# Kernel optimization log

Hardware: AMD Instinct MI355X
Metric: run time of the kernel (lower is better)

Reference implementation:

```python
import jax, jax.numpy as jnp
import numpy as np
from jax import lax

IN_FEATURES = 8192
OUT_FEATURES = 28672


def _unpack3(qweight, infeatures):
    """Unpack GPTQ-style 3-bit weights.

    qweight: (infeatures//32*3, O) int32. Every 3 consecutive int32 rows hold
    32 packed 3-bit values per column (GPTQ quant.py packing): values 0-9 in
    word0 bits [0..30), value 10 split over word0[30:32]|word1[0:1],
    values 11-20 in word1 bits [1..31), value 21 split over word1[31:32]|word2[0:2],
    values 22-31 in word2 bits [2..32).
    Returns float32 (infeatures, O) with raw quant codes in [0, 8).
    """
    O = qweight.shape[1]
    G = infeatures // 32
    q = lax.bitcast_convert_type(qweight, jnp.uint32).reshape(G, 3, O)
    w0, w1, w2 = q[:, 0], q[:, 1], q[:, 2]
    sh = jnp.arange(10, dtype=jnp.uint32)  # 10 whole values per word
    v0 = (w0[:, None, :] >> (3 * sh)[None, :, None]) & 7          # (G,10,O)
    v10 = (((w0 >> 30) & 3) | ((w1 & 1) << 2))[:, None, :]        # (G,1,O)
    v1 = (w1[:, None, :] >> (3 * sh + 1)[None, :, None]) & 7       # (G,10,O)
    v21 = (((w1 >> 31) & 1) | ((w2 & 3) << 1))[:, None, :]        # (G,1,O)
    v2 = (w2[:, None, :] >> (3 * sh + 2)[None, :, None]) & 7       # (G,10,O)
    vals = jnp.concatenate([v0, v10, v1, v21, v2], axis=1)        # (G,32,O)
    return vals.reshape(infeatures, O).astype(jnp.float32)


def setup_inputs() -> dict:
    key = jax.random.key(0)
    k1, k2, k3, k4, k5 = jax.random.split(key, 5)
    x = jax.random.normal(k1, (1, IN_FEATURES), dtype=jnp.float32)
    qweight = jax.random.randint(k2, (IN_FEATURES // 32 * 3, OUT_FEATURES), 0, 2147483647, dtype=jnp.int32)
    scales = jax.random.uniform(k3, (OUT_FEATURES, 1), dtype=jnp.float32)
    zeros = jax.random.normal(k4, (OUT_FEATURES, 1), dtype=jnp.float32)
    bias = jax.random.normal(k5, (OUT_FEATURES,), dtype=jnp.float32)
    return {"x": x, "qweight": qweight, "scales": scales, "zeros": zeros, "bias": bias}


def reference(x, qweight, scales, zeros, bias):
    infeatures = x.shape[-1]
    q = _unpack3(qweight, infeatures)            # (K, O) float codes
    # per-output-channel dequant: W[k, o] = scales[o] * q[k, o] - zeros[o]
    W = scales.T * q - zeros.T                   # (K, O)
    y = x @ W + bias                             # (1, O)
    return y
```

## Files before the change

kernel.cpp:

```cpp
#include <hip/hip_runtime.h>
#include <stdint.h>


typedef float v2f __attribute__((ext_vector_type(2)));

constexpr int O_FEAT  = 28672;
constexpr int IN_FEAT = 8192;
constexpr int NGROUP  = IN_FEAT / 32;
constexpr int SPLIT   = 32;
constexpr int GPB     = NGROUP / SPLIT;
constexpr int O4      = O_FEAT / 4;

__device__ __forceinline__ void dot_group_pk(uint32_t w0, uint32_t w1, uint32_t w2,
                                             const v2f xv[16], v2f& acc) {
  v2f a0 = acc, a1 = {0.f, 0.f};
  #pragma unroll
  for (int t = 0; t < 5; ++t) {
    v2f q = { (float)((w0 >> (6 * t)) & 7u), (float)((w0 >> (6 * t + 3)) & 7u) };
    (t & 1 ? a1 : a0) += xv[t] * q;
  }
  {
    v2f q = { (float)((w0 >> 30) | ((w1 & 1u) << 2)), (float)((w1 >> 1) & 7u) };
    a1 += xv[5] * q;
  }
  #pragma unroll
  for (int t = 0; t < 4; ++t) {
    v2f q = { (float)((w1 >> (4 + 6 * t)) & 7u), (float)((w1 >> (7 + 6 * t)) & 7u) };
    (t & 1 ? a1 : a0) += xv[6 + t] * q;
  }
  {
    v2f q = { (float)((w1 >> 28) & 7u), (float)((w1 >> 31) | ((w2 & 3u) << 1)) };
    a0 += xv[10] * q;
  }
  #pragma unroll
  for (int t = 0; t < 5; ++t) {
    v2f q = { (float)((w2 >> (2 + 6 * t)) & 7u), (float)((w2 >> (5 + 6 * t)) & 7u) };
    (t & 1 ? a1 : a0) += xv[11 + t] * q;
  }
  acc = a0 + a1;
}

__global__ __launch_bounds__(64) void q3_partial(const float* __restrict__ x,
                                                 const uint4* __restrict__ qw4,
                                                 float* __restrict__ part,
                                                 float* __restrict__ partS) {
  const int tcol4 = blockIdx.x * 64 + threadIdx.x;
  const int g0    = blockIdx.y * GPB;
  const uint4* qp = qw4 + (size_t)(3 * g0) * O4 + tcol4;

  __shared__ float xs[GPB * 32];
  const float4 xt = reinterpret_cast<const float4*>(x + g0 * 32)[threadIdx.x];
  reinterpret_cast<float4*>(xs)[threadIdx.x] = xt;

  if (blockIdx.x == 0) {
    float s = (xt.x + xt.y) + (xt.z + xt.w);
    #pragma unroll
    for (int off = 32; off > 0; off >>= 1) s += __shfl_down(s, off, 64);
    if (threadIdx.x == 0) partS[blockIdx.y] = s;
  }

  v2f acc0 = {0.f, 0.f}, acc1 = {0.f, 0.f}, acc2 = {0.f, 0.f}, acc3 = {0.f, 0.f};

  uint4 na = qp[0], nb = qp[O4], nc = qp[2 * O4];
  for (int g = 0; g < GPB; ++g) {
    const uint4 wa = na, wb = nb, wc = nc;
    qp += (g < GPB - 1) ? 3 * O4 : 0;
    na = qp[0]; nb = qp[O4]; nc = qp[2 * O4];

    v2f xv[16];
    const float4* s4 = reinterpret_cast<const float4*>(&xs[g * 32]);
    #pragma unroll
    for (int u = 0; u < 8; ++u) {
      float4 t = s4[u];
      xv[2 * u]     = v2f{t.x, t.y};
      xv[2 * u + 1] = v2f{t.z, t.w};
    }

    dot_group_pk(wa.x, wb.x, wc.x, xv, acc0);
    dot_group_pk(wa.y, wb.y, wc.y, xv, acc1);
    dot_group_pk(wa.z, wb.z, wc.z, xv, acc2);
    dot_group_pk(wa.w, wb.w, wc.w, xv, acc3);
  }

  float4 r = make_float4(acc0.x + acc0.y, acc1.x + acc1.y,
                         acc2.x + acc2.y, acc3.x + acc3.y);
  reinterpret_cast<float4*>(part)[(size_t)blockIdx.y * O4 + tcol4] = r;
}

__global__ __launch_bounds__(256) void q3_finish(const float* __restrict__ part,
                                                 const float* __restrict__ partS,
                                                 const float* __restrict__ scales,
                                                 const float* __restrict__ zeros,
                                                 const float* __restrict__ bias,
                                                 float* __restrict__ out) {
  const int q  = threadIdx.x >> 6;
  const int ol = threadIdx.x & 63;
  const int o  = blockIdx.x * 64 + ol;

  float S = 0.f;
  #pragma unroll
  for (int i = 0; i < 8; ++i) {
    float4 t = reinterpret_cast<const float4*>(partS)[i];
    S += (t.x + t.y) + (t.z + t.w);
  }

  float s0 = 0.f, s1 = 0.f;
  #pragma unroll
  for (int y = 0; y < 8; y += 2) {
    s0 += part[(size_t)(8 * q + y)     * O_FEAT + o];
    s1 += part[(size_t)(8 * q + y + 1) * O_FEAT + o];
  }
  __shared__ float red[4][64];
  red[q][ol] = s0 + s1;
  __syncthreads();
  if (q == 0) {
    float tot = (red[0][ol] + red[1][ol]) + (red[2][ol] + red[3][ol]);
    out[o] = scales[o] * tot - zeros[o] * S + bias[o];
  }
}

extern "C" void kernel_launch(void* const* d_in, const int* in_sizes, int n_in,
                              void* d_out, int out_size, void* d_ws, size_t ws_size,
                              hipStream_t stream) {
  const float* x      = (const float*)d_in[0];
  const uint4* qw4    = (const uint4*)d_in[1];
  const float* scales = (const float*)d_in[2];
  const float* zeros  = (const float*)d_in[3];
  const float* bias   = (const float*)d_in[4];
  float*       out    = (float*)d_out;
  float*       part   = (float*)d_ws;
  float*       partS  = (float*)d_ws + (size_t)SPLIT * O_FEAT;

  q3_partial<<<dim3(O_FEAT / (64 * 4), SPLIT), dim3(64), 0, stream>>>(x, qw4, part, partS);
  q3_finish<<<dim3(O_FEAT / 64), dim3(256), 0, stream>>>(part, partS, scales, zeros, bias, out);
}
```

Baseline: 143.0 us.

## Fuse split-K reduction into partial kernel via last-block atomic counter

```diff
diff --git a/kernel.cpp b/kernel.cpp
--- a/kernel.cpp
+++ b/kernel.cpp
@@ -10,6 +10,7 @@
 constexpr int SPLIT   = 32;
 constexpr int GPB     = NGROUP / SPLIT;
 constexpr int O4      = O_FEAT / 4;
+constexpr int NBX     = O4 / 64;
 
 __device__ __forceinline__ void dot_group_pk(uint32_t w0, uint32_t w1, uint32_t w2,
                                              const v2f xv[16], v2f& acc) {
@@ -40,10 +41,14 @@
   acc = a0 + a1;
 }
 
-__global__ __launch_bounds__(64) void q3_partial(const float* __restrict__ x,
-                                                 const uint4* __restrict__ qw4,
-                                                 float* __restrict__ part,
-                                                 float* __restrict__ partS) {
+__global__ __launch_bounds__(64) void q3_fused(const float* __restrict__ x,
+                                               const uint4* __restrict__ qw4,
+                                               float* __restrict__ part,
+                                               uint32_t* __restrict__ cnt,
+                                               const float* __restrict__ scales,
+                                               const float* __restrict__ zeros,
+                                               const float* __restrict__ bias,
+                                               float* __restrict__ out) {
   const int tcol4 = blockIdx.x * 64 + threadIdx.x;
   const int g0    = blockIdx.y * GPB;
   const uint4* qp = qw4 + (size_t)(3 * g0) * O4 + tcol4;
@@ -51,13 +56,6 @@
   __shared__ float xs[GPB * 32];
   const float4 xt = reinterpret_cast<const float4*>(x + g0 * 32)[threadIdx.x];
   reinterpret_cast<float4*>(xs)[threadIdx.x] = xt;
-
-  if (blockIdx.x == 0) {
-    float s = (xt.x + xt.y) + (xt.z + xt.w);
-    #pragma unroll
-    for (int off = 32; off > 0; off >>= 1) s += __shfl_down(s, off, 64);
-    if (threadIdx.x == 0) partS[blockIdx.y] = s;
-  }
 
   v2f acc0 = {0.f, 0.f}, acc1 = {0.f, 0.f}, acc2 = {0.f, 0.f}, acc3 = {0.f, 0.f};
 
@@ -85,38 +83,52 @@
   float4 r = make_float4(acc0.x + acc0.y, acc1.x + acc1.y,
                          acc2.x + acc2.y, acc3.x + acc3.y);
   reinterpret_cast<float4*>(part)[(size_t)blockIdx.y * O4 + tcol4] = r;
-}
 
-__global__ __launch_bounds__(256) void q3_finish(const float* __restrict__ part,
-                                                 const float* __restrict__ partS,
-                                                 const float* __restrict__ scales,
-                                                 const float* __restrict__ zeros,
-                                                 const float* __restrict__ bias,
-                                                 float* __restrict__ out) {
-  const int q  = threadIdx.x >> 6;
-  const int ol = threadIdx.x & 63;
-  const int o  = blockIdx.x * 64 + ol;
+  __threadfence();
+  uint32_t old = 0;
+  if (threadIdx.x == 0) old = atomicAdd(&cnt[blockIdx.x], 1u);
+  old = (uint32_t)__shfl((int)old, 0, 64);
+  if (old != SPLIT - 1) return;
+  __threadfence();
 
-  float S = 0.f;
+  float s = 0.f;
+  const float4* xall = reinterpret_cast<const float4*>(x);
   #pragma unroll
-  for (int i = 0; i < 8; ++i) {
-    float4 t = reinterpret_cast<const float4*>(partS)[i];
-    S += (t.x + t.y) + (t.z + t.w);
+  for (int i = 0; i < (IN_FEAT / 4) / 64; ++i) {
+    float4 t = xall[i * 64 + threadIdx.x];
+    s += (t.x + t.y) + (t.z + t.w);
   }
+  #pragma unroll
+  for (int off = 32; off > 0; off >>= 1) s += __shfl_xor(s, off, 64);
+  const float S = s;
 
-  float s0 = 0.f, s1 = 0.f;
+  const float4* p4 = reinterpret_cast<const float4*>(part);
+  float4 t0 = {0.f, 0.f, 0.f, 0.f}, t1 = t0, t2 = t0, t3 = t0;
   #pragma unroll
-  for (int y = 0; y < 8; y += 2) {
-    s0 += part[(size_t)(8 * q + y)     * O_FEAT + o];
-    s1 += part[(size_t)(8 * q + y + 1) * O_FEAT + o];
+  for (int y = 0; y < SPLIT; y += 4) {
+    float4 a = p4[(size_t)(y + 0) * O4 + tcol4];
+    float4 b = p4[(size_t)(y + 1) * O4 + tcol4];
+    float4 c = p4[(size_t)(y + 2) * O4 + tcol4];
+    float4 d = p4[(size_t)(y + 3) * O4 + tcol4];
+    t0.x += a.x; t0.y += a.y; t0.z += a.z; t0.w += a.w;
+    t1.x += b.x; t1.y += b.y; t1.z += b.z; t1.w += b.w;
+    t2.x += c.x; t2.y += c.y; t2.z += c.z; t2.w += c.w;
+    t3.x += d.x; t3.y += d.y; t3.z += d.z; t3.w += d.w;
   }
-  __shared__ float red[4][64];
-  red[q][ol] = s0 + s1;
-  __syncthreads();
-  if (q == 0) {
-    float tot = (red[0][ol] + red[1][ol]) + (red[2][ol] + red[3][ol]);
-    out[o] = scales[o] * tot - zeros[o] * S + bias[o];
-  }
+  float4 sum = make_float4((t0.x + t1.x) + (t2.x + t3.x),
+                           (t0.y + t1.y) + (t2.y + t3.y),
+                           (t0.z + t1.z) + (t2.z + t3.z),
+                           (t0.w + t1.w) + (t2.w + t3.w));
+
+  const float4 sc = reinterpret_cast<const float4*>(scales)[tcol4];
+  const float4 zr = reinterpret_cast<const float4*>(zeros)[tcol4];
+  const float4 bi = reinterpret_cast<const float4*>(bias)[tcol4];
+  float4 o;
+  o.x = sc.x * sum.x - zr.x * S + bi.x;
+  o.y = sc.y * sum.y - zr.y * S + bi.y;
+  o.z = sc.z * sum.z - zr.z * S + bi.z;
+  o.w = sc.w * sum.w - zr.w * S + bi.w;
+  reinterpret_cast<float4*>(out)[tcol4] = o;
 }
 
 extern "C" void kernel_launch(void* const* d_in, const int* in_sizes, int n_in,
@@ -129,8 +141,9 @@
   const float* bias   = (const float*)d_in[4];
   float*       out    = (float*)d_out;
   float*       part   = (float*)d_ws;
-  float*       partS  = (float*)d_ws + (size_t)SPLIT * O_FEAT;
+  uint32_t*    cnt    = (uint32_t*)((float*)d_ws + (size_t)SPLIT * O_FEAT);
 
-  q3_partial<<<dim3(O_FEAT / (64 * 4), SPLIT), dim3(64), 0, stream>>>(x, qw4, part, partS);
-  q3_finish<<<dim3(O_FEAT / 64), dim3(256), 0, stream>>>(part, partS, scales, zeros, bias, out);
+  hipMemsetAsync(cnt, 0, NBX * sizeof(uint32_t), stream);
+  q3_fused<<<dim3(NBX, SPLIT), dim3(64), 0, stream>>>(x, qw4, part, cnt,
+                                                      scales, zeros, bias, out);
 }
```

New measurement: 276.5 us. 1.93x slower.
